# Kernel optimization log

Hardware: AMD Instinct MI355X
Metric: run time of the kernel (lower is better)

## Reference

```python
import jax, jax.numpy as jnp
import numpy as np

N = 100000   # num_nodes
F_IN = 128   # num_features
D = 64       # encoder_dim
E = 1600000  # num raw edges (avg degree 16)
BETA = 0.01  # perturb_value


def setup_inputs() -> dict:
    key = jax.random.key(0)
    ks = jax.random.split(key, 8)
    x = jax.random.normal(ks[0], (N, F_IN), dtype=jnp.float32)
    edge_index = jax.random.randint(ks[1], (2, E), 0, N, dtype=jnp.int64)
    W1 = jax.random.normal(ks[2], (F_IN, D), dtype=jnp.float32) * 0.05
    b1 = jnp.zeros((D,), dtype=jnp.float32)
    W2 = jax.random.normal(ks[3], (D, D), dtype=jnp.float32) * 0.05
    b2 = jnp.zeros((D,), dtype=jnp.float32)
    # torch FloatTensor(...).normal_(-beta, beta): mean=-beta, std=beta
    perturb1 = jax.random.normal(ks[4], (N, D), dtype=jnp.float32) * BETA - BETA
    perturb2 = jax.random.normal(ks[5], (N, D), dtype=jnp.float32) * BETA - BETA
    return {"x": x, "edge_index": edge_index, "W1": W1, "b1": b1,
            "W2": W2, "b2": b2, "perturb1": perturb1, "perturb2": perturb2}


def _graph_conv(h, src, dst, norm, W, b):
    # linear transform then gather -> weighted message -> scatter-add
    h = h @ W                                  # [N, D]
    msg = h[src] * norm[:, None]               # [E+N, D] irregular gather
    agg = jax.ops.segment_sum(msg, dst, num_segments=N)  # scatter-add
    return agg + b


def reference(x, edge_index, W1, b1, W2, b2, perturb1, perturb2):
    # add self-loops (GCN/PPMI-style propagation with symmetric norm;
    # PPMI edge weights approximated by degree normalization)
    loops = jnp.arange(N, dtype=edge_index.dtype)
    src = jnp.concatenate([edge_index[0], loops])
    dst = jnp.concatenate([edge_index[1], loops])
    deg = jax.ops.segment_sum(jnp.ones_like(dst, dtype=x.dtype), dst, num_segments=N)
    deg = jnp.maximum(deg, 1.0)
    norm = jax.lax.rsqrt(deg[src] * deg[dst])  # [E+N]

    h = _graph_conv(x, src, dst, norm, W1, b1) + perturb1
    h = jax.nn.relu(h)                         # dropout = identity (eval mode)
    h = _graph_conv(h, src, dst, norm, W2, b2) + perturb2
    return h
```

## Files before the change

kernel.cpp:

```cpp
#include <hip/hip_runtime.h>

#define DD 64
#define FIN 128
#define BK 256
#define MAXBUK 512
#define CAP 8192
#define ESCAP 12288
#define EPB 4096

typedef _Float16 half8 __attribute__((ext_vector_type(8)));
typedef _Float16 h2 __attribute__((ext_vector_type(2)));
typedef float f32x4 __attribute__((ext_vector_type(4)));

union U4 { uint4 u; h2 h[4]; };

__global__ __launch_bounds__(256) void k_bucket(const int* __restrict__ src,
                                                const int* __restrict__ dst,
                                                unsigned* __restrict__ buf,
                                                int* __restrict__ gcur,
                                                int E, int nbuk) {
    __shared__ int hist[MAXBUK];
    __shared__ int base[MAXBUK];
    int e0 = blockIdx.x * EPB;
    int e1 = min(e0 + EPB, E);
    int dreg[16];
#pragma unroll
    for (int i = 0; i < 16; ++i) {
        int e = e0 + threadIdx.x + i * 256;
        dreg[i] = (e < e1) ? dst[e] : -1;
    }
    for (int i = threadIdx.x; i < nbuk; i += 256) hist[i] = 0;
    __syncthreads();
#pragma unroll
    for (int i = 0; i < 16; ++i)
        if (dreg[i] >= 0) atomicAdd(&hist[dreg[i] >> 8], 1);
    __syncthreads();
    for (int i = threadIdx.x; i < nbuk; i += 256) {
        int c = hist[i];
        base[i] = c ? atomicAdd(&gcur[i], c) : 0;
        hist[i] = 0;
    }
    __syncthreads();
#pragma unroll
    for (int i = 0; i < 16; ++i) {
        int d = dreg[i];
        if (d >= 0) {
            int e = e0 + threadIdx.x + i * 256;
            int b = d >> 8;
            int off = base[b] + atomicAdd(&hist[b], 1);
            if (off < CAP)
                buf[(size_t)b * CAP + off] = ((unsigned)src[e] << 8) | ((unsigned)d & 255u);
        }
    }
}

__global__ __launch_bounds__(256) void k_csr(const unsigned* __restrict__ buf,
                                             const int* __restrict__ gcur,
                                             int* __restrict__ rowptr,
                                             int* __restrict__ lenp,
                                             float* __restrict__ rs,
                                             int* __restrict__ es, int n, int dummy) {
    __shared__ int cnt[BK];
    __shared__ int excl[BK];
    __shared__ int cur[BK];
    __shared__ int wsum[4];
    int b = blockIdx.x;
    int tid = threadIdx.x;
    int lane = tid & 63, wid = tid >> 6;
    cnt[tid] = 0;
    cur[tid] = 0;
    __syncthreads();
    int count = gcur[b];
    const unsigned* rec = buf + (size_t)b * CAP;
    for (int i = tid; i < count; i += 256)
        atomicAdd(&cnt[rec[i] & (BK - 1)], 1);
    __syncthreads();
    int v = cnt[tid];
    int pv = (v + 15) & ~15;
    int s = pv;
    for (int off = 1; off < 64; off <<= 1) {
        int t = __shfl_up(s, off, 64);
        if (lane >= off) s += t;
    }
    if (lane == 63) wsum[wid] = s;
    __syncthreads();
    int wo = 0;
    for (int w = 0; w < wid; ++w) wo += wsum[w];
    excl[tid] = s - pv + wo;
    __syncthreads();
    int node = b * BK + tid;
    int base = b * ESCAP;
    if (node < n) {
        rowptr[node] = base + excl[tid];
        lenp[node] = pv;
        rs[node] = rsqrtf((float)(v + 1));
    }
    for (int i = tid; i < count; i += 256) {
        unsigned r = rec[i];
        int local = r & (BK - 1);
        int pos = base + excl[local] + atomicAdd(&cur[local], 1);
        es[pos] = (int)(r >> 8);
    }
    int st = base + excl[tid];
    for (int i = v; i < pv; ++i) es[st + i] = dummy;
}

__global__ __launch_bounds__(256) void k_prep(const float* __restrict__ W1,
                                              const float* __restrict__ W2,
                                              _Float16* __restrict__ Wt1,
                                              _Float16* __restrict__ Wt2,
                                              int* __restrict__ gcur) {
    int tid = threadIdx.x;
    gcur[tid] = 0;
    gcur[tid + 256] = 0;
    for (int i = tid; i < FIN * DD; i += 256) {
        int k = i >> 6, c = i & 63;
        Wt1[c * FIN + k] = (_Float16)W1[i];
    }
    for (int i = tid; i < DD * DD; i += 256) {
        int k = i >> 6, c = i & 63;
        Wt2[c * DD + k] = (_Float16)W2[i];
    }
}

__global__ __launch_bounds__(256) void k_gemm1(const float* __restrict__ x,
                                               const _Float16* __restrict__ Wt,
                                               const float* __restrict__ rs,
                                               _Float16* __restrict__ hpf, int n) {
    __shared__ _Float16 sx[64 * 136];
    int row0 = blockIdx.x * 64;
    int tid = threadIdx.x;
    for (int i = tid; i < 2048; i += 256) {
        int r = i >> 5, c = i & 31;
        int row = row0 + r;
        float4 v = make_float4(0.f, 0.f, 0.f, 0.f);
        if (row < n) v = *(const float4*)(x + (size_t)row * FIN + c * 4);
        union { _Float16 h[4]; uint2 u; } t;
        t.h[0] = (_Float16)v.x; t.h[1] = (_Float16)v.y;
        t.h[2] = (_Float16)v.z; t.h[3] = (_Float16)v.w;
        *(uint2*)(sx + r * 136 + c * 4) = t.u;
    }
    __syncthreads();
    int lane = tid & 63, wave = tid >> 6;
    int r15 = lane & 15, g = lane >> 4;
    half8 a[4];
    const _Float16* ap = sx + (wave * 16 + r15) * 136 + g * 8;
#pragma unroll
    for (int kc = 0; kc < 4; ++kc) a[kc] = *(const half8*)(ap + kc * 32);
    half8 bfr[4][4];
    const _Float16* bp = Wt + (size_t)r15 * FIN + g * 8;
#pragma unroll
    for (int ct = 0; ct < 4; ++ct)
#pragma unroll
        for (int kc = 0; kc < 4; ++kc)
            bfr[ct][kc] = *(const half8*)(bp + ct * 16 * FIN + kc * 32);
    f32x4 acc[4] = {{0.f,0.f,0.f,0.f},{0.f,0.f,0.f,0.f},{0.f,0.f,0.f,0.f},{0.f,0.f,0.f,0.f}};
#pragma unroll
    for (int ct = 0; ct < 4; ++ct)
#pragma unroll
        for (int kc = 0; kc < 4; ++kc)
            acc[ct] = __builtin_amdgcn_mfma_f32_16x16x32_f16(a[kc], bfr[ct][kc], acc[ct], 0, 0, 0);
    __syncthreads();
#pragma unroll
    for (int reg = 0; reg < 4; ++reg) {
        int rowl = wave * 16 + g * 4 + reg;
        int row = row0 + rowl;
        float sc = (row < n) ? rs[row] : 0.f;
#pragma unroll
        for (int ct = 0; ct < 4; ++ct)
            sx[rowl * 72 + ct * 16 + r15] = (_Float16)(acc[ct][reg] * sc);
    }
    __syncthreads();
    for (int i = tid; i < 1024; i += 256) {
        int r = i >> 4, q = i & 15;
        uint2 v = *(const uint2*)(sx + r * 72 + q * 4);
        *(uint2*)(hpf + (size_t)(row0 + r) * DD + q * 4) = v;
    }
}

__global__ __launch_bounds__(256) void k_gemm2(const _Float16* __restrict__ ain,
                                               const _Float16* __restrict__ Wt,
                                               const float* __restrict__ rs,
                                               _Float16* __restrict__ hpf, int n) {
    __shared__ _Float16 sx[64 * 72];
    int row0 = blockIdx.x * 64;
    int tid = threadIdx.x;
    for (int i = tid; i < 512; i += 256) {
        int r = i >> 3, c = i & 7;
        int row = row0 + r;
        uint4 v = make_uint4(0u, 0u, 0u, 0u);
        if (row < n) v = *(const uint4*)(ain + (size_t)row * DD + c * 8);
        *(uint4*)(sx + r * 72 + c * 8) = v;
    }
    __syncthreads();
    int lane = tid & 63, wave = tid >> 6;
    int r15 = lane & 15, g = lane >> 4;
    half8 a[2];
    const _Float16* ap = sx + (wave * 16 + r15) * 72 + g * 8;
#pragma unroll
    for (int kc = 0; kc < 2; ++kc) a[kc] = *(const half8*)(ap + kc * 32);
    half8 bfr[4][2];
    const _Float16* bp = Wt + (size_t)r15 * DD + g * 8;
#pragma unroll
    for (int ct = 0; ct < 4; ++ct)
#pragma unroll
        for (int kc = 0; kc < 2; ++kc)
            bfr[ct][kc] = *(const half8*)(bp + ct * 16 * DD + kc * 32);
    f32x4 acc[4] = {{0.f,0.f,0.f,0.f},{0.f,0.f,0.f,0.f},{0.f,0.f,0.f,0.f},{0.f,0.f,0.f,0.f}};
#pragma unroll
    for (int ct = 0; ct < 4; ++ct)
#pragma unroll
        for (int kc = 0; kc < 2; ++kc)
            acc[ct] = __builtin_amdgcn_mfma_f32_16x16x32_f16(a[kc], bfr[ct][kc], acc[ct], 0, 0, 0);
    __syncthreads();
#pragma unroll
    for (int reg = 0; reg < 4; ++reg) {
        int rowl = wave * 16 + g * 4 + reg;
        int row = row0 + rowl;
        float sc = (row < n) ? rs[row] : 0.f;
#pragma unroll
        for (int ct = 0; ct < 4; ++ct)
            sx[rowl * 72 + ct * 16 + r15] = (_Float16)(acc[ct][reg] * sc);
    }
    __syncthreads();
    for (int i = tid; i < 1024; i += 256) {
        int r = i >> 4, q = i & 15;
        uint2 v = *(const uint2*)(sx + r * 72 + q * 4);
        *(uint2*)(hpf + (size_t)(row0 + r) * DD + q * 4) = v;
    }
}

template <bool F16OUT>
__global__ __launch_bounds__(256) void k_agg(const uint4* __restrict__ hp4,
                                             const int* __restrict__ es,
                                             const int* __restrict__ rowptr,
                                             const int* __restrict__ lenp,
                                             const float* __restrict__ rs,
                                             const float* __restrict__ b,
                                             const float* __restrict__ pert,
                                             float* __restrict__ outp,
                                             _Float16* __restrict__ outh, int n) {
    int lane = threadIdx.x & 63;
    int wv = threadIdx.x >> 6;
    int q = lane & 7;
    int g = lane >> 3;
    int node = (blockIdx.x * 4 + wv) * 8 + g;
    bool alive = node < n;
    int nc = alive ? node : 0;
    int e0 = rowptr[nc];
    int len = alive ? lenp[nc] : 0;
    int nbt = len >> 4;
    float r = rs[nc];
    size_t o = (size_t)nc * DD + q * 8;
    float4 p0 = *(const float4*)(pert + o);
    float4 p1 = *(const float4*)(pert + o + 4);
    float4 b0 = *(const float4*)(b + q * 8);
    float4 b1 = *(const float4*)(b + q * 8 + 4);
    h2 A[4] = {{0,0},{0,0},{0,0},{0,0}};
    h2 B[4] = {{0,0},{0,0},{0,0},{0,0}};
    h2 C[4] = {{0,0},{0,0},{0,0},{0,0}};
    h2 D[4] = {{0,0},{0,0},{0,0},{0,0}};
    {
        U4 t; t.u = hp4[(size_t)nc * 8 + q];
        A[0] += t.h[0]; A[1] += t.h[1]; A[2] += t.h[2]; A[3] += t.h[3];
    }
    for (int t = 0; t < nbt; ++t) {
        uint2 eb = *(const uint2*)(es + e0 + t * 16 + q * 2);
        int j0  = __shfl((int)eb.x, 0, 8), j1  = __shfl((int)eb.y, 0, 8);
        int j2  = __shfl((int)eb.x, 1, 8), j3  = __shfl((int)eb.y, 1, 8);
        int j4  = __shfl((int)eb.x, 2, 8), j5  = __shfl((int)eb.y, 2, 8);
        int j6  = __shfl((int)eb.x, 3, 8), j7  = __shfl((int)eb.y, 3, 8);
        int j8  = __shfl((int)eb.x, 4, 8), j9  = __shfl((int)eb.y, 4, 8);
        int j10 = __shfl((int)eb.x, 5, 8), j11 = __shfl((int)eb.y, 5, 8);
        int j12 = __shfl((int)eb.x, 6, 8), j13 = __shfl((int)eb.y, 6, 8);
        int j14 = __shfl((int)eb.x, 7, 8), j15 = __shfl((int)eb.y, 7, 8);
        U4 v0, v1, v2, v3, v4, v5, v6, v7, v8, v9, v10, v11, v12, v13, v14, v15;
        v0.u  = hp4[(size_t)j0  * 8 + q];
        v1.u  = hp4[(size_t)j1  * 8 + q];
        v2.u  = hp4[(size_t)j2  * 8 + q];
        v3.u  = hp4[(size_t)j3  * 8 + q];
        v4.u  = hp4[(size_t)j4  * 8 + q];
        v5.u  = hp4[(size_t)j5  * 8 + q];
        v6.u  = hp4[(size_t)j6  * 8 + q];
        v7.u  = hp4[(size_t)j7  * 8 + q];
        v8.u  = hp4[(size_t)j8  * 8 + q];
        v9.u  = hp4[(size_t)j9  * 8 + q];
        v10.u = hp4[(size_t)j10 * 8 + q];
        v11.u = hp4[(size_t)j11 * 8 + q];
        v12.u = hp4[(size_t)j12 * 8 + q];
        v13.u = hp4[(size_t)j13 * 8 + q];
        v14.u = hp4[(size_t)j14 * 8 + q];
        v15.u = hp4[(size_t)j15 * 8 + q];
#pragma unroll
        for (int k = 0; k < 4; ++k) {
            A[k] += v0.h[k];  B[k] += v1.h[k];  C[k] += v2.h[k];  D[k] += v3.h[k];
            A[k] += v4.h[k];  B[k] += v5.h[k];  C[k] += v6.h[k];  D[k] += v7.h[k];
            A[k] += v8.h[k];  B[k] += v9.h[k];  C[k] += v10.h[k]; D[k] += v11.h[k];
            A[k] += v12.h[k]; B[k] += v13.h[k]; C[k] += v14.h[k]; D[k] += v15.h[k];
        }
    }
    if (alive) {
        float F[8];
#pragma unroll
        for (int k = 0; k < 4; ++k) {
            F[2 * k]     = ((float)A[k].x + (float)B[k].x) + ((float)C[k].x + (float)D[k].x);
            F[2 * k + 1] = ((float)A[k].y + (float)B[k].y) + ((float)C[k].y + (float)D[k].y);
        }
        float r0 = fmaf(r, F[0], b0.x + p0.x);
        float r1 = fmaf(r, F[1], b0.y + p0.y);
        float r2 = fmaf(r, F[2], b0.z + p0.z);
        float r3 = fmaf(r, F[3], b0.w + p0.w);
        float r4 = fmaf(r, F[4], b1.x + p1.x);
        float r5 = fmaf(r, F[5], b1.y + p1.y);
        float r6 = fmaf(r, F[6], b1.z + p1.z);
        float r7 = fmaf(r, F[7], b1.w + p1.w);
        if (F16OUT) {
            union { _Float16 h[8]; uint4 u; } t;
            t.h[0] = (_Float16)fmaxf(r0, 0.f);
            t.h[1] = (_Float16)fmaxf(r1, 0.f);
            t.h[2] = (_Float16)fmaxf(r2, 0.f);
            t.h[3] = (_Float16)fmaxf(r3, 0.f);
            t.h[4] = (_Float16)fmaxf(r4, 0.f);
            t.h[5] = (_Float16)fmaxf(r5, 0.f);
            t.h[6] = (_Float16)fmaxf(r6, 0.f);
            t.h[7] = (_Float16)fmaxf(r7, 0.f);
            *(uint4*)(outh + o) = t.u;
        } else {
            *(float4*)(outp + o) = make_float4(r0, r1, r2, r3);
            *(float4*)(outp + o + 4) = make_float4(r4, r5, r6, r7);
        }
    }
}

extern "C" void kernel_launch(void* const* d_in, const int* in_sizes, int n_in,
                              void* d_out, int out_size, void* d_ws, size_t ws_size,
                              hipStream_t stream) {
    const float* x  = (const float*)d_in[0];
    const int*   ei = (const int*)d_in[1];
    const float* W1 = (const float*)d_in[2];
    const float* b1 = (const float*)d_in[3];
    const float* W2 = (const float*)d_in[4];
    const float* b2 = (const float*)d_in[5];
    const float* p1 = (const float*)d_in[6];
    const float* p2 = (const float*)d_in[7];
    float* out = (float*)d_out;

    int n = in_sizes[0] / FIN;
    int E = in_sizes[1] / 2;
    const int* src = ei;
    const int* dst = ei + E;
    int nbuk = (n + BK - 1) / BK;
    int gb = (n + 63) / 64;

    char* ws = (char*)d_ws;
    size_t off = 0;
    int* gcur   = (int*)(ws + off); off += sizeof(int) * MAXBUK;
    int* rowptr = (int*)(ws + off); off += sizeof(int) * (size_t)n;
    int* lenp   = (int*)(ws + off); off += sizeof(int) * (size_t)n;
    float* rs   = (float*)(ws + off); off += sizeof(float) * (size_t)n;
    int* es     = (int*)(ws + off); off += sizeof(int) * (size_t)nbuk * ESCAP;
    off = (off + 15) & ~(size_t)15;
    unsigned* buf = (unsigned*)(ws + off);
    off += sizeof(unsigned) * (size_t)nbuk * CAP;
    off = (off + 15) & ~(size_t)15;
    _Float16* hpf = (_Float16*)(ws + off);
    off += (size_t)gb * 64 * DD * 2;
    off = (off + 15) & ~(size_t)15;
    _Float16* hpf2 = (_Float16*)(ws + off);
    off += (size_t)gb * 64 * DD * 2;
    off = (off + 15) & ~(size_t)15;
    _Float16* Wt1 = (_Float16*)(ws + off); off += FIN * DD * 2;
    _Float16* Wt2 = (_Float16*)(ws + off); off += DD * DD * 2;

    int ab = (n + 31) / 32;
    int bb = (E + EPB - 1) / EPB;

    k_prep<<<1, 256, 0, stream>>>(W1, W2, Wt1, Wt2, gcur);
    k_bucket<<<bb, 256, 0, stream>>>(src, dst, buf, gcur, E, nbuk);
    k_csr<<<nbuk, 256, 0, stream>>>(buf, gcur, rowptr, lenp, rs, es, n, n);

    k_gemm1<<<gb, 256, 0, stream>>>(x, Wt1, rs, hpf, n);
    k_agg<true><<<ab, 256, 0, stream>>>((const uint4*)hpf, es, rowptr, lenp, rs,
                                        b1, p1, nullptr, hpf2, n);
    k_gemm2<<<gb, 256, 0, stream>>>(hpf2, Wt2, rs, hpf, n);
    k_agg<false><<<ab, 256, 0, stream>>>((const uint4*)hpf, es, rowptr, lenp, rs,
                                         b2, p2, out, nullptr, n);
}
```

Measured before the change: 168.9 us.

## Split feature columns into two halves for cache-resident gather aggregation

The GEMM outputs are written as two column-split fp16 arrays of 32 features each, and each aggregation layer now runs as two passes, one per half. Each node is handled by 4 lanes instead of 8. The gathered table per pass is halved (about 6.4 MB), so the random neighbor gathers are more likely to hit in L2/MALL. The cost is that edge indices, rowptr and normalisation are read twice and two extra kernels are launched.

```diff
diff --git a/kernel.cpp b/kernel.cpp
--- a/kernel.cpp
+++ b/kernel.cpp
@@ -126,7 +126,8 @@
 __global__ __launch_bounds__(256) void k_gemm1(const float* __restrict__ x,
                                                const _Float16* __restrict__ Wt,
                                                const float* __restrict__ rs,
-                                               _Float16* __restrict__ hpf, int n) {
+                                               _Float16* __restrict__ hpA,
+                                               _Float16* __restrict__ hpB, int n) {
     __shared__ _Float16 sx[64 * 136];
     int row0 = blockIdx.x * 64;
     int tid = threadIdx.x;
@@ -174,22 +175,27 @@
     for (int i = tid; i < 1024; i += 256) {
         int r = i >> 4, q = i & 15;
         uint2 v = *(const uint2*)(sx + r * 72 + q * 4);
-        *(uint2*)(hpf + (size_t)(row0 + r) * DD + q * 4) = v;
-    }
-}
-
-__global__ __launch_bounds__(256) void k_gemm2(const _Float16* __restrict__ ain,
+        if (q < 8) *(uint2*)(hpA + (size_t)(row0 + r) * 32 + q * 4) = v;
+        else       *(uint2*)(hpB + (size_t)(row0 + r) * 32 + (q - 8) * 4) = v;
+    }
+}
+
+__global__ __launch_bounds__(256) void k_gemm2(const _Float16* __restrict__ ainA,
+                                               const _Float16* __restrict__ ainB,
                                                const _Float16* __restrict__ Wt,
                                                const float* __restrict__ rs,
-                                               _Float16* __restrict__ hpf, int n) {
+                                               _Float16* __restrict__ hpA,
+                                               _Float16* __restrict__ hpB, int n) {
     __shared__ _Float16 sx[64 * 72];
     int row0 = blockIdx.x * 64;
     int tid = threadIdx.x;
+    const uint4* A4 = (const uint4*)ainA;
+    const uint4* B4 = (const uint4*)ainB;
     for (int i = tid; i < 512; i += 256) {
         int r = i >> 3, c = i & 7;
         int row = row0 + r;
         uint4 v = make_uint4(0u, 0u, 0u, 0u);
-        if (row < n) v = *(const uint4*)(ain + (size_t)row * DD + c * 8);
+        if (row < n) v = (c < 4) ? A4[(size_t)row * 4 + c] : B4[(size_t)row * 4 + (c - 4)];
         *(uint4*)(sx + r * 72 + c * 8) = v;
     }
     __syncthreads();
@@ -226,7 +232,8 @@
     for (int i = tid; i < 1024; i += 256) {
         int r = i >> 4, q = i & 15;
         uint2 v = *(const uint2*)(sx + r * 72 + q * 4);
-        *(uint2*)(hpf + (size_t)(row0 + r) * DD + q * 4) = v;
+        if (q < 8) *(uint2*)(hpA + (size_t)(row0 + r) * 32 + q * 4) = v;
+        else       *(uint2*)(hpB + (size_t)(row0 + r) * 32 + (q - 8) * 4) = v;
     }
 }
 
@@ -239,58 +246,59 @@
                                              const float* __restrict__ b,
                                              const float* __restrict__ pert,
                                              float* __restrict__ outp,
-                                             _Float16* __restrict__ outh, int n) {
+                                             _Float16* __restrict__ outh,
+                                             int colbase, int n) {
     int lane = threadIdx.x & 63;
     int wv = threadIdx.x >> 6;
-    int q = lane & 7;
-    int g = lane >> 3;
-    int node = (blockIdx.x * 4 + wv) * 8 + g;
+    int q = lane & 3;
+    int g = lane >> 2;
+    int node = (blockIdx.x * 4 + wv) * 16 + g;
     bool alive = node < n;
     int nc = alive ? node : 0;
     int e0 = rowptr[nc];
     int len = alive ? lenp[nc] : 0;
     int nbt = len >> 4;
     float r = rs[nc];
-    size_t o = (size_t)nc * DD + q * 8;
-    float4 p0 = *(const float4*)(pert + o);
-    float4 p1 = *(const float4*)(pert + o + 4);
-    float4 b0 = *(const float4*)(b + q * 8);
-    float4 b1 = *(const float4*)(b + q * 8 + 4);
+    size_t op = (size_t)nc * DD + colbase + q * 8;
+    float4 p0 = *(const float4*)(pert + op);
+    float4 p1 = *(const float4*)(pert + op + 4);
+    float4 b0 = *(const float4*)(b + colbase + q * 8);
+    float4 b1 = *(const float4*)(b + colbase + q * 8 + 4);
     h2 A[4] = {{0,0},{0,0},{0,0},{0,0}};
     h2 B[4] = {{0,0},{0,0},{0,0},{0,0}};
     h2 C[4] = {{0,0},{0,0},{0,0},{0,0}};
     h2 D[4] = {{0,0},{0,0},{0,0},{0,0}};
     {
-        U4 t; t.u = hp4[(size_t)nc * 8 + q];
+        U4 t; t.u = hp4[(size_t)nc * 4 + q];
         A[0] += t.h[0]; A[1] += t.h[1]; A[2] += t.h[2]; A[3] += t.h[3];
     }
     for (int t = 0; t < nbt; ++t) {
-        uint2 eb = *(const uint2*)(es + e0 + t * 16 + q * 2);
-        int j0  = __shfl((int)eb.x, 0, 8), j1  = __shfl((int)eb.y, 0, 8);
-        int j2  = __shfl((int)eb.x, 1, 8), j3  = __shfl((int)eb.y, 1, 8);
-        int j4  = __shfl((int)eb.x, 2, 8), j5  = __shfl((int)eb.y, 2, 8);
-        int j6  = __shfl((int)eb.x, 3, 8), j7  = __shfl((int)eb.y, 3, 8);
-        int j8  = __shfl((int)eb.x, 4, 8), j9  = __shfl((int)eb.y, 4, 8);
-        int j10 = __shfl((int)eb.x, 5, 8), j11 = __shfl((int)eb.y, 5, 8);
-        int j12 = __shfl((int)eb.x, 6, 8), j13 = __shfl((int)eb.y, 6, 8);
-        int j14 = __shfl((int)eb.x, 7, 8), j15 = __shfl((int)eb.y, 7, 8);
+        uint4 eb = *(const uint4*)(es + e0 + t * 16 + q * 4);
+        int j0  = __shfl((int)eb.x, 0, 4), j1  = __shfl((int)eb.y, 0, 4);
+        int j2  = __shfl((int)eb.z, 0, 4), j3  = __shfl((int)eb.w, 0, 4);
+        int j4  = __shfl((int)eb.x, 1, 4), j5  = __shfl((int)eb.y, 1, 4);
+        int j6  = __shfl((int)eb.z, 1, 4), j7  = __shfl((int)eb.w, 1, 4);
+        int j8  = __shfl((int)eb.x, 2, 4), j9  = __shfl((int)eb.y, 2, 4);
+        int j10 = __shfl((int)eb.z, 2, 4), j11 = __shfl((int)eb.w, 2, 4);
+        int j12 = __shfl((int)eb.x, 3, 4), j13 = __shfl((int)eb.y, 3, 4);
+        int j14 = __shfl((int)eb.z, 3, 4), j15 = __shfl((int)eb.w, 3, 4);
         U4 v0, v1, v2, v3, v4, v5, v6, v7, v8, v9, v10, v11, v12, v13, v14, v15;
-        v0.u  = hp4[(size_t)j0  * 8 + q];
-        v1.u  = hp4[(size_t)j1  * 8 + q];
-        v2.u  = hp4[(size_t)j2  * 8 + q];
-        v3.u  = hp4[(size_t)j3  * 8 + q];
-        v4.u  = hp4[(size_t)j4  * 8 + q];
-        v5.u  = hp4[(size_t)j5  * 8 + q];
-        v6.u  = hp4[(size_t)j6  * 8 + q];
-        v7.u  = hp4[(size_t)j7  * 8 + q];
-        v8.u  = hp4[(size_t)j8  * 8 + q];
-        v9.u  = hp4[(size_t)j9  * 8 + q];
-        v10.u = hp4[(size_t)j10 * 8 + q];
-        v11.u = hp4[(size_t)j11 * 8 + q];
-        v12.u = hp4[(size_t)j12 * 8 + q];
-        v13.u = hp4[(size_t)j13 * 8 + q];
-        v14.u = hp4[(size_t)j14 * 8 + q];
-        v15.u = hp4[(size_t)j15 * 8 + q];
+        v0.u  = hp4[(size_t)j0  * 4 + q];
+        v1.u  = hp4[(size_t)j1  * 4 + q];
+        v2.u  = hp4[(size_t)j2  * 4 + q];
+        v3.u  = hp4[(size_t)j3  * 4 + q];
+        v4.u  = hp4[(size_t)j4  * 4 + q];
+        v5.u  = hp4[(size_t)j5  * 4 + q];
+        v6.u  = hp4[(size_t)j6  * 4 + q];
+        v7.u  = hp4[(size_t)j7  * 4 + q];
+        v8.u  = hp4[(size_t)j8  * 4 + q];
+        v9.u  = hp4[(size_t)j9  * 4 + q];
+        v10.u = hp4[(size_t)j10 * 4 + q];
+        v11.u = hp4[(size_t)j11 * 4 + q];
+        v12.u = hp4[(size_t)j12 * 4 + q];
+        v13.u = hp4[(size_t)j13 * 4 + q];
+        v14.u = hp4[(size_t)j14 * 4 + q];
+        v15.u = hp4[(size_t)j15 * 4 + q];
 #pragma unroll
         for (int k = 0; k < 4; ++k) {
             A[k] += v0.h[k];  B[k] += v1.h[k];  C[k] += v2.h[k];  D[k] += v3.h[k];
@@ -324,10 +332,10 @@
             t.h[5] = (_Float16)fmaxf(r5, 0.f);
             t.h[6] = (_Float16)fmaxf(r6, 0.f);
             t.h[7] = (_Float16)fmaxf(r7, 0.f);
-            *(uint4*)(outh + o) = t.u;
+            *(uint4*)(outh + (size_t)nc * 32 + q * 8) = t.u;
         } else {
-            *(float4*)(outp + o) = make_float4(r0, r1, r2, r3);
-            *(float4*)(outp + o + 4) = make_float4(r4, r5, r6, r7);
+            *(float4*)(outp + op) = make_float4(r0, r1, r2, r3);
+            *(float4*)(outp + op + 4) = make_float4(r4, r5, r6, r7);
         }
     }
 }
@@ -362,27 +370,31 @@
     off = (off + 15) & ~(size_t)15;
     unsigned* buf = (unsigned*)(ws + off);
     off += sizeof(unsigned) * (size_t)nbuk * CAP;
+    size_t half_bytes = (size_t)gb * 64 * 32 * 2;
     off = (off + 15) & ~(size_t)15;
-    _Float16* hpf = (_Float16*)(ws + off);
-    off += (size_t)gb * 64 * DD * 2;
-    off = (off + 15) & ~(size_t)15;
-    _Float16* hpf2 = (_Float16*)(ws + off);
-    off += (size_t)gb * 64 * DD * 2;
+    _Float16* hpA = (_Float16*)(ws + off); off += half_bytes;
+    _Float16* hpB = (_Float16*)(ws + off); off += half_bytes;
+    _Float16* h2A = (_Float16*)(ws + off); off += half_bytes;
+    _Float16* h2B = (_Float16*)(ws + off); off += half_bytes;
     off = (off + 15) & ~(size_t)15;
     _Float16* Wt1 = (_Float16*)(ws + off); off += FIN * DD * 2;
     _Float16* Wt2 = (_Float16*)(ws + off); off += DD * DD * 2;
 
-    int ab = (n + 31) / 32;
+    int ab = (n + 63) / 64;
     int bb = (E + EPB - 1) / EPB;
 
     k_prep<<<1, 256, 0, stream>>>(W1, W2, Wt1, Wt2, gcur);
     k_bucket<<<bb, 256, 0, stream>>>(src, dst, buf, gcur, E, nbuk);
     k_csr<<<nbuk, 256, 0, stream>>>(buf, gcur, rowptr, lenp, rs, es, n, n);
 
-    k_gemm1<<<gb, 256, 0, stream>>>(x, Wt1, rs, hpf, n);
-    k_agg<true><<<ab, 256, 0, stream>>>((const uint4*)hpf, es, rowptr, lenp, rs,
-                                        b1, p1, nullptr, hpf2, n);
-    k_gemm2<<<gb, 256, 0, stream>>>(hpf2, Wt2, rs, hpf, n);
-    k_agg<false><<<ab, 256, 0, stream>>>((const uint4*)hpf, es, rowptr, lenp, rs,
-                                         b2, p2, out, nullptr, n);
-}
+    k_gemm1<<<gb, 256, 0, stream>>>(x, Wt1, rs, hpA, hpB, n);
+    k_agg<true><<<ab, 256, 0, stream>>>((const uint4*)hpA, es, rowptr, lenp, rs,
+                                        b1, p1, nullptr, h2A, 0, n);
+    k_agg<true><<<ab, 256, 0, stream>>>((const uint4*)hpB, es, rowptr, lenp, rs,
+                                        b1, p1, nullptr, h2B, 32, n);
+    k_gemm2<<<gb, 256, 0, stream>>>(h2A, h2B, Wt2, rs, hpA, hpB, n);
+    k_agg<false><<<ab, 256, 0, stream>>>((const uint4*)hpA, es, rowptr, lenp, rs,
+                                         b2, p2, out, nullptr, 0, n);
+    k_agg<false><<<ab, 256, 0, stream>>>((const uint4*)hpB, es, rowptr, lenp, rs,
+                                         b2, p2, out, nullptr, 32, n);
+}
```

New measurement: 186.6 us. 1.1x slower.
